# Optimization experiments

Measured on AMD Instinct MI355X. Metric: run time of the kernel, lower is better.

## Reference

```python
import jax, jax.numpy as jnp
import numpy as np

DIM = 256
D_STATE = 64
D_CONV = 4
EXPAND = 2
D_INNER = EXPAND * DIM          # 512
DT_RANK = DIM // 16             # 16, Mamba default dt_rank='auto'
LN_EPS = 1e-5


def setup_inputs() -> dict:
    key = jax.random.key(0)
    ks = jax.random.split(key, 8)
    B, L = 4, 1024
    s = lambda k, shape, fan: jax.random.normal(k, shape, jnp.float32) / np.sqrt(fan).astype(np.float32)
    inp = {}
    inp['x'] = jax.random.normal(ks[0], (B, L, DIM), jnp.float32)
    inp['C_SA'] = jax.random.normal(ks[1], (B, L, D_STATE), jnp.float32)
    # LayerNorm params
    inp['gamma'] = jnp.ones((DIM,), jnp.float32)
    inp['beta'] = jnp.zeros((DIM,), jnp.float32)
    # Mamba params
    inp['W_in'] = s(ks[2], (2 * D_INNER, DIM), DIM)
    inp['conv_w'] = s(ks[3], (D_INNER, 1, D_CONV), D_CONV)   # depthwise causal conv
    inp['conv_b'] = jnp.zeros((D_INNER,), jnp.float32)
    inp['W_x'] = s(ks[4], (DT_RANK + D_STATE, D_INNER), D_INNER)  # -> (dt_low_rank, B_ssm)
    inp['W_dt'] = s(ks[5], (D_INNER, DT_RANK), DT_RANK)
    # softplus-inverse of 0.01 so initial dt ~ 0.01 (Mamba dt init)
    inp['b_dt'] = jnp.log(jnp.expm1(jnp.full((D_INNER,), 0.01, jnp.float32)))
    # S4D-real init: A = -[1..N]
    inp['A_log'] = jnp.log(jnp.broadcast_to(jnp.arange(1, D_STATE + 1, dtype=jnp.float32), (D_INNER, D_STATE)))
    inp['D'] = jnp.ones((D_INNER,), jnp.float32)
    inp['W_out'] = s(ks[6], (DIM, D_INNER), D_INNER)
    return inp


def reference(x, C_SA, gamma, beta, W_in, conv_w, conv_b, W_x, W_dt, b_dt, A_log, D, W_out):
    B, L, _ = x.shape
    # --- LayerNorm ---
    mu = jnp.mean(x, axis=-1, keepdims=True)
    var = jnp.mean(jnp.square(x - mu), axis=-1, keepdims=True)
    xn = (x - mu) * jax.lax.rsqrt(var + LN_EPS) * gamma + beta
    # --- input projection and gate split ---
    xz = xn @ W_in.T                              # [B,L,2*Di]
    u, z = jnp.split(xz, 2, axis=-1)
    # --- causal depthwise conv1d + SiLU ---
    u_c = jax.lax.conv_general_dilated(
        u.transpose(0, 2, 1), conv_w, (1,), [(D_CONV - 1, 0)],
        feature_group_count=D_INNER,
        dimension_numbers=('NCH', 'OIH', 'NCH'))  # [B,Di,L]
    u = jax.nn.silu(u_c.transpose(0, 2, 1) + conv_b)  # [B,L,Di]
    # --- data-dependent SSM params (C comes from C_SA externally) ---
    dbl = u @ W_x.T                               # [B,L,dt_rank+N]
    dt = jax.nn.softplus(dbl[..., :DT_RANK] @ W_dt.T + b_dt)  # [B,L,Di]
    Bs = dbl[..., DT_RANK:]                       # [B,L,N]
    A = -jnp.exp(A_log)                           # [Di,N]
    # --- selective scan over time ---
    def step(h, t):
        dt_t, B_t, C_t, u_t = t                   # [B,Di],[B,N],[B,N],[B,Di]
        dA = jnp.exp(dt_t[..., None] * A)         # [B,Di,N]
        h = dA * h + (dt_t * u_t)[..., None] * B_t[:, None, :]
        y = jnp.einsum('bdn,bn->bd', h, C_t)
        return h, y
    h0 = jnp.zeros((B, D_INNER, D_STATE), x.dtype)
    xs = (dt.transpose(1, 0, 2), Bs.transpose(1, 0, 2),
          C_SA.transpose(1, 0, 2), u.transpose(1, 0, 2))
    _, ys = jax.lax.scan(step, h0, xs)            # ys: [L,B,Di]
    y = ys.transpose(1, 0, 2) + u * D             # skip connection
    y = y * jax.nn.silu(z)                        # gate
    return y @ W_out.T                            # [B,L,dim]
```

## Files before the change

### kernel.cpp

```cpp
#include <hip/hip_runtime.h>
#include <cstdint>
#include <cstddef>

#define B_    4
#define L_    1024
#define DIM_  256
#define DI_   512
#define NTOK  (B_*L_)
#define NC    32
#define CL    (L_/NC)

__device__ __forceinline__ float siluf_(float x){ return x / (1.0f + __expf(-x)); }
__device__ __forceinline__ float softplusf_(float x){
  return (x > 15.0f) ? x : log1pf(__expf(x));
}

__global__ __launch_bounds__(1024) void k_check(const float* __restrict__ A_log,
    int* __restrict__ flag){
  __shared__ int s_ok;
  int tid = threadIdx.x;
  if (tid == 0) s_ok = 1;
  __syncthreads();
  int ok = 1;
  for (int i = tid; i < 512 * 64; i += 1024){
    int n = i & 63;
    float ref = logf((float)(n + 1));
    float v = A_log[i];
    if (fabsf(v - ref) > 1e-5f * fmaxf(1.0f, fabsf(ref))) ok = 0;
  }
  if (!ok) atomicAnd(&s_ok, 0);
  __syncthreads();
  if (tid == 0) *flag = s_ok;
}

__global__ __launch_bounds__(256) void k_ln_stats(const float* __restrict__ x,
    float* __restrict__ stats){
  int tok  = blockIdx.x * 4 + (threadIdx.x >> 6);
  int lane = threadIdx.x & 63;
  float4 v = *(const float4*)(x + (size_t)tok * DIM_ + lane * 4);
  float s  = v.x + v.y + v.z + v.w;
  float sq = v.x*v.x + v.y*v.y + v.z*v.z + v.w*v.w;
  #pragma unroll
  for (int off = 32; off; off >>= 1){
    s  += __shfl_xor(s,  off, 64);
    sq += __shfl_xor(sq, off, 64);
  }
  if (lane == 0){
    float mu = s * (1.0f / DIM_);
    stats[tok*2]   = mu;
    stats[tok*2+1] = rsqrtf(sq * (1.0f / DIM_) - mu*mu + 1e-5f);
  }
}

__global__ __launch_bounds__(256) void k_gemm1(const float* __restrict__ x,
    const float* __restrict__ stats, const float* __restrict__ gamma,
    const float* __restrict__ beta, const float* __restrict__ Win,
    float* __restrict__ xz){
  __shared__ float As[16 * 68];
  __shared__ float Bs[16 * 68];
  int tid = threadIdx.x;
  int mBase = blockIdx.y * 64;
  int nBase = blockIdx.x * 64;
  int tx = tid & 15, ty = tid >> 4;
  int am = tid >> 2, ak = (tid & 3) << 2;
  float mu = stats[(mBase+am)*2], rs = stats[(mBase+am)*2+1];
  float acc[4][4] = {};
  const float* xp = x   + (size_t)(mBase+am)*256 + ak;
  const float* wp = Win + (size_t)(nBase+am)*256 + ak;
  float4 av = *(const float4*)(xp);
  float4 bv = *(const float4*)(wp);
  float4 gv = *(const float4*)(gamma + ak);
  float4 be = *(const float4*)(beta  + ak);
  for (int kt = 0; kt < 256; kt += 16){
    As[(ak+0)*68+am] = (av.x - mu) * rs * gv.x + be.x;
    As[(ak+1)*68+am] = (av.y - mu) * rs * gv.y + be.y;
    As[(ak+2)*68+am] = (av.z - mu) * rs * gv.z + be.z;
    As[(ak+3)*68+am] = (av.w - mu) * rs * gv.w + be.w;
    Bs[(ak+0)*68+am]=bv.x; Bs[(ak+1)*68+am]=bv.y;
    Bs[(ak+2)*68+am]=bv.z; Bs[(ak+3)*68+am]=bv.w;
    __syncthreads();
    float4 avN, bvN, gvN, beN;
    if (kt + 16 < 256){
      avN = *(const float4*)(xp + kt + 16);
      bvN = *(const float4*)(wp + kt + 16);
      gvN = *(const float4*)(gamma + kt + 16 + ak);
      beN = *(const float4*)(beta  + kt + 16 + ak);
    }
    #pragma unroll
    for (int kk = 0; kk < 16; kk++){
      float4 a = *(const float4*)&As[kk*68 + ty*4];
      float4 b = *(const float4*)&Bs[kk*68 + tx*4];
      float ar[4] = {a.x,a.y,a.z,a.w}, br[4] = {b.x,b.y,b.z,b.w};
      #pragma unroll
      for (int i=0;i<4;i++)
        #pragma unroll
        for (int j=0;j<4;j++)
          acc[i][j] += ar[i]*br[j];
    }
    __syncthreads();
    av = avN; bv = bvN; gv = gvN; be = beN;
  }
  #pragma unroll
  for (int i=0;i<4;i++){
    float4 o = make_float4(acc[i][0],acc[i][1],acc[i][2],acc[i][3]);
    *(float4*)(xz + (size_t)(mBase+ty*4+i)*1024 + nBase + tx*4) = o;
  }
}

__global__ __launch_bounds__(256) void k_conv(const float* __restrict__ xz,
    const float* __restrict__ cw, const float* __restrict__ cb,
    float* __restrict__ uc){
  int g = blockIdx.x * 256 + threadIdx.x;
  int d = g & 511;
  int tok = g >> 9;
  int t = tok & (L_ - 1);
  float w0 = cw[d*4+0], w1 = cw[d*4+1], w2 = cw[d*4+2], w3 = cw[d*4+3];
  const float* up = xz + (size_t)tok * 1024 + d;
  float acc = cb[d] + w3 * up[0];
  if (t >= 1) acc += w2 * up[-1 * 1024];
  if (t >= 2) acc += w1 * up[-2 * 1024];
  if (t >= 3) acc += w0 * up[-3 * 1024];
  uc[g] = siluf_(acc);
}

__global__ __launch_bounds__(320) void k_gemm2(const float* __restrict__ uc,
    const float* __restrict__ Wx, float* __restrict__ dbl){
  __shared__ float As[4 * 516];
  int tid = threadIdx.x;
  int mBase = blockIdx.x * 4;
  for (int idx = tid * 4; idx < 4 * 512; idx += 320 * 4){
    int r = idx >> 9, k = idx & 511;
    *(float4*)&As[r * 516 + k] = *(const float4*)(uc + (size_t)(mBase + r) * 512 + k);
  }
  __syncthreads();
  int n = tid >> 2;
  int r = tid & 3;
  const float* arow = &As[r * 516];
  const float* wp = Wx + (size_t)n * 512;
  float acc = 0.f;
  #pragma unroll 8
  for (int k4 = 0; k4 < 512; k4 += 4){
    float4 a = *(const float4*)&arow[k4];
    float4 w = *(const float4*)(wp + k4);
    acc += a.x*w.x + a.y*w.y + a.z*w.z + a.w*w.w;
  }
  dbl[(size_t)(mBase + r) * 80 + n] = acc;
}

__global__ __launch_bounds__(256) void k_dt(const float* __restrict__ dbl,
    const float* __restrict__ Wdt, const float* __restrict__ bdt,
    float* __restrict__ dt){
  int g = blockIdx.x * 256 + threadIdx.x;
  int d = g & 511; int m = g >> 9;
  float acc = bdt[d];
  const float* r = dbl + (size_t)m * 80;
  #pragma unroll
  for (int k = 0; k < 16; k++)
    acc += r[k] * Wdt[d * 16 + k];
  dt[g] = softplusf_(acc);
}

__global__ __launch_bounds__(256, 4) void k_scanA(const float* __restrict__ dt,
    const float* __restrict__ uc, const float* __restrict__ dbl,
    const float* __restrict__ A_log, const int* __restrict__ flagp,
    float* __restrict__ hseg, float* __restrict__ S){
  __shared__ float sB[CL][64];
  __shared__ float sDt[CL][32];
  __shared__ float sU[CL][32];
  int tid  = threadIdx.x;
  int gw   = (blockIdx.x * 256 + tid) >> 6;
  int lane = tid & 63;
  int dsub = lane & 7, ngrp = lane >> 3;
  int grp = gw & 255;
  int c   = gw >> 8;
  int ch  = grp * 8 + dsub;
  int b = ch >> 9, d = ch & 511;
  int tbeg = c * CL;
  int ch0 = ((blockIdx.x * 4) & 255) * 8;
  int d0  = ch0 & 511;
  {
    const float* Bsrc = dbl + (size_t)b * L_ * 80 + (size_t)tbeg * 80 + 16;
    for (int i = tid; i < CL * 16; i += 256){
      int row = i >> 4, col = (i & 15) << 2;
      *(float4*)&sB[row][col] = *(const float4*)(Bsrc + row * 80 + col);
    }
    const float* Dsrc = dt + (size_t)b * L_ * 512 + (size_t)tbeg * 512 + d0;
    const float* Usrc = uc + (size_t)b * L_ * 512 + (size_t)tbeg * 512 + d0;
    int zr = tid >> 3, zc = (tid & 7) << 2;
    *(float4*)&sDt[zr][zc] = *(const float4*)(Dsrc + zr * 512 + zc);
    *(float4*)&sU[zr][zc]  = *(const float4*)(Usrc + zr * 512 + zc);
  }
  __syncthreads();
  int fast = *flagp;
  int lch = (grp & 3) * 8 + dsub;
  float h[8] = {};
  float Ssum = 0.f;
  float st1 = (float)(ngrp * 8 + 1);
  if (fast){
    for (int tt = 0; tt < CL; tt += 4){
      #pragma unroll
      for (int j = 0; j < 4; j++){
        float dtv = sDt[tt+j][lch];
        float uv  = sU[tt+j][lch];
        float4 b0 = *(const float4*)&sB[tt+j][ngrp*8];
        float4 b1 = *(const float4*)&sB[tt+j][ngrp*8+4];
        float sc = dtv * uv;
        Ssum += dtv;
        float e1 = __expf(-dtv);
        float e2 = e1 * e1;
        float e4 = e2 * e2;
        float dA0 = __expf(-dtv * st1);
        float dA1 = dA0 * e1;
        float dA2 = dA0 * e2;
        float dA3 = dA1 * e2;
        h[0] = dA0 * h[0] + sc * b0.x;
        h[1] = dA1 * h[1] + sc * b0.y;
        h[2] = dA2 * h[2] + sc * b0.z;
        h[3] = dA3 * h[3] + sc * b0.w;
        dA0 *= e4; dA1 *= e4; dA2 *= e4; dA3 *= e4;
        h[4] = dA0 * h[4] + sc * b1.x;
        h[5] = dA1 * h[5] + sc * b1.y;
        h[6] = dA2 * h[6] + sc * b1.z;
        h[7] = dA3 * h[7] + sc * b1.w;
      }
    }
  } else {
    float Aa[8];
    float4 a0 = *(const float4*)(A_log + (size_t)d*64 + ngrp*8);
    float4 a1 = *(const float4*)(A_log + (size_t)d*64 + ngrp*8 + 4);
    Aa[0]=-__expf(a0.x); Aa[1]=-__expf(a0.y); Aa[2]=-__expf(a0.z); Aa[3]=-__expf(a0.w);
    Aa[4]=-__expf(a1.x); Aa[5]=-__expf(a1.y); Aa[6]=-__expf(a1.z); Aa[7]=-__expf(a1.w);
    for (int tt = 0; tt < CL; tt += 4){
      #pragma unroll
      for (int j = 0; j < 4; j++){
        float dtv = sDt[tt+j][lch];
        float uv  = sU[tt+j][lch];
        float4 b0 = *(const float4*)&sB[tt+j][ngrp*8];
        float4 b1 = *(const float4*)&sB[tt+j][ngrp*8+4];
        float Bv[8] = {b0.x,b0.y,b0.z,b0.w,b1.x,b1.y,b1.z,b1.w};
        float sc = dtv * uv;
        Ssum += dtv;
        #pragma unroll
        for (int i = 0; i < 8; i++)
          h[i] = __expf(dtv * Aa[i]) * h[i] + sc * Bv[i];
      }
    }
  }
  float* hp = hseg + ((size_t)(c * 2048 + ch)) * 64 + ngrp*8;
  *(float4*)hp     = make_float4(h[0],h[1],h[2],h[3]);
  *(float4*)(hp+4) = make_float4(h[4],h[5],h[6],h[7]);
  if (ngrp == 0) S[c * 2048 + ch] = Ssum;
}

__global__ __launch_bounds__(256) void k_scanB(float* __restrict__ hseg,
    const float* __restrict__ S, const float* __restrict__ A_log,
    const int* __restrict__ flagp){
  int ch   = (blockIdx.x * 256 + threadIdx.x) >> 6;
  int lane = threadIdx.x & 63;
  int d = ch & 511;
  int fast = *flagp;
  float A = fast ? -(float)(lane + 1) : -__expf(A_log[(size_t)d * 64 + lane]);
  float hc = 0.f;
  #pragma unroll 8
  for (int c = 0; c < NC; c++){
    size_t idx = ((size_t)(c * 2048 + ch)) * 64 + lane;
    float hf = hseg[idx];
    hseg[idx] = hc;
    float Sv = S[c * 2048 + ch];
    hc = hf + __expf(A * Sv) * hc;
  }
}

__global__ __launch_bounds__(256, 4) void k_scanC(const float* __restrict__ dt,
    const float* __restrict__ uc, const float* __restrict__ dbl,
    const float* __restrict__ C_SA, const float* __restrict__ A_log,
    const int* __restrict__ flagp,
    const float* __restrict__ hin, const float* __restrict__ xz,
    const float* __restrict__ Dp, float* __restrict__ ys){
  __shared__ float sB[CL][64];
  __shared__ float sC[CL][64];
  __shared__ float sZ[CL][32];
  __shared__ float sDt[CL][32];
  __shared__ float sU[CL][32];
  int tid  = threadIdx.x;
  int gw   = (blockIdx.x * 256 + tid) >> 6;
  int lane = tid & 63;
  int dsub = lane & 7, ngrp = lane >> 3;
  int grp = gw & 255;
  int c   = gw >> 8;
  int ch  = grp * 8 + dsub;
  int b = ch >> 9, d = ch & 511;
  int tbeg = c * CL;
  int ch0 = ((blockIdx.x * 4) & 255) * 8;
  int d0  = ch0 & 511;
  {
    const float* Bsrc = dbl  + (size_t)b * L_ * 80 + (size_t)tbeg * 80 + 16;
    const float* Csrc = C_SA + (size_t)b * L_ * 64 + (size_t)tbeg * 64;
    for (int i = tid; i < CL * 16; i += 256){
      int row = i >> 4, col = (i & 15) << 2;
      *(float4*)&sB[row][col] = *(const float4*)(Bsrc + row * 80 + col);
      *(float4*)&sC[row][col] = *(const float4*)(Csrc + row * 64 + col);
    }
    const float* Zsrc = xz + (size_t)b * L_ * 1024 + (size_t)tbeg * 1024 + 512 + d0;
    const float* Dsrc = dt + (size_t)b * L_ * 512 + (size_t)tbeg * 512 + d0;
    const float* Usrc = uc + (size_t)b * L_ * 512 + (size_t)tbeg * 512 + d0;
    int zr = tid >> 3, zc = (tid & 7) << 2;
    *(float4*)&sZ[zr][zc]  = *(const float4*)(Zsrc + zr * 1024 + zc);
    *(float4*)&sDt[zr][zc] = *(const float4*)(Dsrc + zr * 512 + zc);
    *(float4*)&sU[zr][zc]  = *(const float4*)(Usrc + zr * 512 + zc);
  }
  __syncthreads();
  int fast = *flagp;
  float Dv = Dp[d];
  int lch = (grp & 3) * 8 + dsub;
  float*       yw  = ys + (size_t)b * L_ * 512 + d;
  float h[8];
  {
    const float* hp = hin + ((size_t)(c * 2048 + ch)) * 64 + ngrp*8;
    float4 h0 = *(const float4*)hp;
    float4 h1 = *(const float4*)(hp + 4);
    h[0]=h0.x; h[1]=h0.y; h[2]=h0.z; h[3]=h0.w;
    h[4]=h1.x; h[5]=h1.y; h[6]=h1.z; h[7]=h1.w;
  }
  float st1 = (float)(ngrp * 8 + 1);
  if (fast){
    for (int tt = 0; tt < CL; tt += 4){
      float yp[4], uj[4];
      #pragma unroll
      for (int j = 0; j < 4; j++){
        float dtv = sDt[tt+j][lch];
        float uv  = sU[tt+j][lch];
        uj[j] = uv;
        float4 b0 = *(const float4*)&sB[tt+j][ngrp*8];
        float4 b1 = *(const float4*)&sB[tt+j][ngrp*8+4];
        float4 c0 = *(const float4*)&sC[tt+j][ngrp*8];
        float4 c1 = *(const float4*)&sC[tt+j][ngrp*8+4];
        float sc = dtv * uv;
        float e1 = __expf(-dtv);
        float e2 = e1 * e1;
        float e4 = e2 * e2;
        float dA0 = __expf(-dtv * st1);
        float dA1 = dA0 * e1;
        float dA2 = dA0 * e2;
        float dA3 = dA1 * e2;
        h[0] = dA0 * h[0] + sc * b0.x;
        h[1] = dA1 * h[1] + sc * b0.y;
        h[2] = dA2 * h[2] + sc * b0.z;
        h[3] = dA3 * h[3] + sc * b0.w;
        float y0 = h[0] * c0.x;
        float y1 = h[1] * c0.y;
        float y2 = h[2] * c0.z;
        float y3 = h[3] * c0.w;
        dA0 *= e4; dA1 *= e4; dA2 *= e4; dA3 *= e4;
        h[4] = dA0 * h[4] + sc * b1.x;
        h[5] = dA1 * h[5] + sc * b1.y;
        h[6] = dA2 * h[6] + sc * b1.z;
        h[7] = dA3 * h[7] + sc * b1.w;
        y0 += h[4] * c1.x;
        y1 += h[5] * c1.y;
        y2 += h[6] * c1.z;
        y3 += h[7] * c1.w;
        yp[j] = (y0 + y1) + (y2 + y3);
      }
      #pragma unroll
      for (int off = 8; off < 64; off <<= 1){
        #pragma unroll
        for (int j = 0; j < 4; j++)
          yp[j] += __shfl_xor(yp[j], off, 64);
      }
      if (ngrp == 0){
        #pragma unroll
        for (int j = 0; j < 4; j++){
          float z = sZ[tt+j][lch];
          yw[(size_t)(tbeg+tt+j) * 512] = (yp[j] + uj[j] * Dv) * siluf_(z);
        }
      }
    }
  } else {
    float Aa[8];
    float4 a0 = *(const float4*)(A_log + (size_t)d*64 + ngrp*8);
    float4 a1 = *(const float4*)(A_log + (size_t)d*64 + ngrp*8 + 4);
    Aa[0]=-__expf(a0.x); Aa[1]=-__expf(a0.y); Aa[2]=-__expf(a0.z); Aa[3]=-__expf(a0.w);
    Aa[4]=-__expf(a1.x); Aa[5]=-__expf(a1.y); Aa[6]=-__expf(a1.z); Aa[7]=-__expf(a1.w);
    for (int tt = 0; tt < CL; tt += 4){
      float yp[4], uj[4];
      #pragma unroll
      for (int j = 0; j < 4; j++){
        float dtv = sDt[tt+j][lch];
        float uv  = sU[tt+j][lch];
        uj[j] = uv;
        float4 b0 = *(const float4*)&sB[tt+j][ngrp*8];
        float4 b1 = *(const float4*)&sB[tt+j][ngrp*8+4];
        float4 c0 = *(const float4*)&sC[tt+j][ngrp*8];
        float4 c1 = *(const float4*)&sC[tt+j][ngrp*8+4];
        float sc = dtv * uv;
        h[0] = __expf(dtv * Aa[0]) * h[0] + sc * b0.x;
        h[1] = __expf(dtv * Aa[1]) * h[1] + sc * b0.y;
        h[2] = __expf(dtv * Aa[2]) * h[2] + sc * b0.z;
        h[3] = __expf(dtv * Aa[3]) * h[3] + sc * b0.w;
        float y0 = h[0] * c0.x;
        float y1 = h[1] * c0.y;
        float y2 = h[2] * c0.z;
        float y3 = h[3] * c0.w;
        h[4] = __expf(dtv * Aa[4]) * h[4] + sc * b1.x;
        h[5] = __expf(dtv * Aa[5]) * h[5] + sc * b1.y;
        h[6] = __expf(dtv * Aa[6]) * h[6] + sc * b1.z;
        h[7] = __expf(dtv * Aa[7]) * h[7] + sc * b1.w;
        y0 += h[4] * c1.x;
        y1 += h[5] * c1.y;
        y2 += h[6] * c1.z;
        y3 += h[7] * c1.w;
        yp[j] = (y0 + y1) + (y2 + y3);
      }
      #pragma unroll
      for (int off = 8; off < 64; off <<= 1){
        #pragma unroll
        for (int j = 0; j < 4; j++)
          yp[j] += __shfl_xor(yp[j], off, 64);
      }
      if (ngrp == 0){
        #pragma unroll
        for (int j = 0; j < 4; j++){
          float z = sZ[tt+j][lch];
          yw[(size_t)(tbeg+tt+j) * 512] = (yp[j] + uj[j] * Dv) * siluf_(z);
        }
      }
    }
  }
}

__global__ __launch_bounds__(256) void k_gemm3s(const float* __restrict__ Ag,
    const float* __restrict__ Wout, float* __restrict__ pbuf){
  __shared__ float As[16 * 68];
  __shared__ float Bs[16 * 68];
  int tid = threadIdx.x;
  int nBase = blockIdx.x * 64;
  int mBase = blockIdx.y * 64;
  int kBase = blockIdx.z * 128;
  int tx = tid & 15, ty = tid >> 4;
  int am = tid >> 2, ak = (tid & 3) << 2;
  float acc[4][4] = {};
  const float* ap = Ag   + (size_t)(mBase+am)*512 + ak;
  const float* wp = Wout + (size_t)(nBase+am)*512 + ak;
  float4 av = *(const float4*)(ap + kBase);
  float4 bv = *(const float4*)(wp + kBase);
  for (int kt = kBase; kt < kBase + 128; kt += 16){
    As[(ak+0)*68+am]=av.x; As[(ak+1)*68+am]=av.y;
    As[(ak+2)*68+am]=av.z; As[(ak+3)*68+am]=av.w;
    Bs[(ak+0)*68+am]=bv.x; Bs[(ak+1)*68+am]=bv.y;
    Bs[(ak+2)*68+am]=bv.z; Bs[(ak+3)*68+am]=bv.w;
    __syncthreads();
    float4 avN, bvN;
    if (kt + 16 < kBase + 128){
      avN = *(const float4*)(ap + kt + 16);
      bvN = *(const float4*)(wp + kt + 16);
    }
    #pragma unroll
    for (int kk = 0; kk < 16; kk++){
      float4 a = *(const float4*)&As[kk*68 + ty*4];
      float4 b = *(const float4*)&Bs[kk*68 + tx*4];
      float ar[4] = {a.x,a.y,a.z,a.w}, br[4] = {b.x,b.y,b.z,b.w};
      #pragma unroll
      for (int i=0;i<4;i++)
        #pragma unroll
        for (int j=0;j<4;j++)
          acc[i][j] += ar[i]*br[j];
    }
    __syncthreads();
    av = avN; bv = bvN;
  }
  float* pw = pbuf + (size_t)blockIdx.z * (NTOK * 256);
  #pragma unroll
  for (int i=0;i<4;i++){
    float4 o = make_float4(acc[i][0],acc[i][1],acc[i][2],acc[i][3]);
    *(float4*)(pw + (size_t)(mBase+ty*4+i)*256 + nBase + tx*4) = o;
  }
}

__global__ __launch_bounds__(256) void k_g3red(const float* __restrict__ pbuf,
    float* __restrict__ out){
  int i4 = (blockIdx.x * 256 + threadIdx.x) * 4;
  float4 a = *(const float4*)(pbuf + i4);
  float4 b = *(const float4*)(pbuf + (size_t)NTOK*256   + i4);
  float4 c = *(const float4*)(pbuf + (size_t)NTOK*512   + i4);
  float4 d = *(const float4*)(pbuf + (size_t)NTOK*768   + i4);
  float4 o = make_float4((a.x+b.x)+(c.x+d.x), (a.y+b.y)+(c.y+d.y),
                         (a.z+b.z)+(c.z+d.z), (a.w+b.w)+(c.w+d.w));
  *(float4*)(out + i4) = o;
}

extern "C" void kernel_launch(void* const* d_in, const int* in_sizes, int n_in,
                              void* d_out, int out_size, void* d_ws, size_t ws_size,
                              hipStream_t stream) {
  const float* x      = (const float*)d_in[0];
  const float* C_SA   = (const float*)d_in[1];
  const float* gamma  = (const float*)d_in[2];
  const float* beta   = (const float*)d_in[3];
  const float* W_in   = (const float*)d_in[4];
  const float* conv_w = (const float*)d_in[5];
  const float* conv_b = (const float*)d_in[6];
  const float* W_x    = (const float*)d_in[7];
  const float* W_dt   = (const float*)d_in[8];
  const float* b_dt   = (const float*)d_in[9];
  const float* A_log  = (const float*)d_in[10];
  const float* Dw     = (const float*)d_in[11];
  const float* W_out  = (const float*)d_in[12];
  float* out = (float*)d_out;

  float* ws    = (float*)d_ws;
  float* stats = ws;
  int*   flag  = (int*)(ws + 8192);
  float* xz    = ws    + 16384;
  float* uc    = xz    + 4194304;
  float* dbl   = uc    + 2097152;
  float* dtb   = dbl   + 327680;
  float* hseg  = dtb   + 2097152;
  float* S     = hseg  + 4194304;
  float* ysb   = S     + 65536;
  float* pbuf  = hseg;

  k_check<<<1, 1024, 0, stream>>>(A_log, flag);
  k_ln_stats<<<NTOK/4, 256, 0, stream>>>(x, stats);
  k_gemm1<<<dim3(16, 64), 256, 0, stream>>>(x, stats, gamma, beta, W_in, xz);
  k_conv <<<(NTOK*512)/256, 256, 0, stream>>>(xz, conv_w, conv_b, uc);
  k_gemm2<<<1024, 320, 0, stream>>>(uc, W_x, dbl);
  k_dt   <<<(NTOK*512)/256, 256, 0, stream>>>(dbl, W_dt, b_dt, dtb);
  k_scanA<<<NC*64, 256, 0, stream>>>(dtb, uc, dbl, A_log, flag, hseg, S);
  k_scanB<<<512, 256, 0, stream>>>(hseg, S, A_log, flag);
  k_scanC<<<NC*64, 256, 0, stream>>>(dtb, uc, dbl, C_SA, A_log, flag, hseg, xz, Dw, ysb);
  k_gemm3s<<<dim3(4, 64, 4), 256, 0, stream>>>(ysb, W_out, pbuf);
  k_g3red<<<NTOK*256/1024, 256, 0, stream>>>(pbuf, out);
}
```

Baseline: 242.8 us.

## Retile x-projection GEMM into register-blocked warp tiles with split-K shuffle reduction

Rewrites the u @ W_x^T kernel so each 64-lane wavefront computes an 8-token by 8-output tile. K is split across 8 lane groups and the partial sums are combined with xor shuffles. The old version staged 4 rows in shared memory and had each thread do a full 512-long dot product while reloading W_x rows from global memory. The new scheme gets register reuse of the activation chunks across 8 outputs and drops shared memory and the barrier, at the cost of higher register pressure and only one lane in eight doing the stores.

```diff
diff --git a/kernel.cpp b/kernel.cpp
--- a/kernel.cpp
+++ b/kernel.cpp
@@ -123,28 +123,48 @@
   uc[g] = siluf_(acc);
 }
 
-__global__ __launch_bounds__(320) void k_gemm2(const float* __restrict__ uc,
+__global__ __launch_bounds__(256) void k_gemm2(const float* __restrict__ uc,
     const float* __restrict__ Wx, float* __restrict__ dbl){
-  __shared__ float As[4 * 516];
-  int tid = threadIdx.x;
-  int mBase = blockIdx.x * 4;
-  for (int idx = tid * 4; idx < 4 * 512; idx += 320 * 4){
-    int r = idx >> 9, k = idx & 511;
-    *(float4*)&As[r * 516 + k] = *(const float4*)(uc + (size_t)(mBase + r) * 512 + k);
-  }
-  __syncthreads();
-  int n = tid >> 2;
-  int r = tid & 3;
-  const float* arow = &As[r * 516];
-  const float* wp = Wx + (size_t)n * 512;
-  float acc = 0.f;
-  #pragma unroll 8
-  for (int k4 = 0; k4 < 512; k4 += 4){
-    float4 a = *(const float4*)&arow[k4];
-    float4 w = *(const float4*)(wp + k4);
-    acc += a.x*w.x + a.y*w.y + a.z*w.z + a.w*w.w;
-  }
-  dbl[(size_t)(mBase + r) * 80 + n] = acc;
+  int tid  = threadIdx.x;
+  int w    = blockIdx.x * 4 + (tid >> 6);
+  int lane = tid & 63;
+  int tg = w / 10;
+  int ng = w - tg * 10;
+  int ts = lane >> 3;
+  int ko = lane & 7;
+  int m  = tg * 8 + ts;
+  const float4* ap = (const float4*)(uc + (size_t)m * 512 + ko * 64);
+  const float*  wb = Wx + (size_t)(ng * 8) * 512 + ko * 64;
+  float pn[8] = {};
+  #pragma unroll
+  for (int half = 0; half < 2; half++){
+    float4 a[8];
+    #pragma unroll
+    for (int i = 0; i < 8; i++) a[i] = ap[half*8 + i];
+    #pragma unroll
+    for (int n = 0; n < 8; n++){
+      const float4* wp = (const float4*)(wb + (size_t)n * 512) + half*8;
+      float4 w0 = wp[0], w1 = wp[1], w2 = wp[2], w3 = wp[3];
+      float4 w4 = wp[4], w5 = wp[5], w6 = wp[6], w7 = wp[7];
+      float s0 = a[0].x*w0.x + a[0].y*w0.y + a[0].z*w0.z + a[0].w*w0.w
+               + a[4].x*w4.x + a[4].y*w4.y + a[4].z*w4.z + a[4].w*w4.w;
+      float s1 = a[1].x*w1.x + a[1].y*w1.y + a[1].z*w1.z + a[1].w*w1.w
+               + a[5].x*w5.x + a[5].y*w5.y + a[5].z*w5.z + a[5].w*w5.w;
+      float s2 = a[2].x*w2.x + a[2].y*w2.y + a[2].z*w2.z + a[2].w*w2.w
+               + a[6].x*w6.x + a[6].y*w6.y + a[6].z*w6.z + a[6].w*w6.w;
+      float s3 = a[3].x*w3.x + a[3].y*w3.y + a[3].z*w3.z + a[3].w*w3.w
+               + a[7].x*w7.x + a[7].y*w7.y + a[7].z*w7.z + a[7].w*w7.w;
+      pn[n] += (s0 + s1) + (s2 + s3);
+    }
+  }
+  #pragma unroll
+  for (int n = 0; n < 8; n++){
+    float p = pn[n];
+    p += __shfl_xor(p, 1, 64);
+    p += __shfl_xor(p, 2, 64);
+    p += __shfl_xor(p, 4, 64);
+    if (ko == 0) dbl[(size_t)m * 80 + ng * 8 + n] = p;
+  }
 }
 
 __global__ __launch_bounds__(256) void k_dt(const float* __restrict__ dbl,
@@ -523,7 +543,7 @@
   k_ln_stats<<<NTOK/4, 256, 0, stream>>>(x, stats);
   k_gemm1<<<dim3(16, 64), 256, 0, stream>>>(x, stats, gamma, beta, W_in, xz);
   k_conv <<<(NTOK*512)/256, 256, 0, stream>>>(xz, conv_w, conv_b, uc);
-  k_gemm2<<<1024, 320, 0, stream>>>(uc, W_x, dbl);
+  k_gemm2<<<1280, 256, 0, stream>>>(uc, W_x, dbl);
   k_dt   <<<(NTOK*512)/256, 256, 0, stream>>>(dbl, W_dt, b_dt, dtb);
   k_scanA<<<NC*64, 256, 0, stream>>>(dtb, uc, dbl, A_log, flag, hseg, S);
   k_scanB<<<512, 256, 0, stream>>>(hseg, S, A_log, flag);
```

New measurement: 327.3 us. 34.8% more time.

## Replace x_proj GEMM with split-K register-tiled kernel plus reduction

Applied to the files above, without the earlier changes.

Replaces the per-row x_proj GEMM, which streamed W_x from global memory for every 4 rows, with a shared-memory tiled kernel. Each thread computes a 4x5 register tile over a 64x80 output tile, and K is split 16 ways across blocks. The partial sums go to a scratch buffer that aliases hseg and are summed by a new reduction kernel. This adds a second launch and roughly 21 MB of partial-sum traffic in exchange for much better reuse of both operands.

```diff
diff --git a/kernel.cpp b/kernel.cpp
--- a/kernel.cpp
+++ b/kernel.cpp
@@ -123,28 +123,62 @@
   uc[g] = siluf_(acc);
 }
 
-__global__ __launch_bounds__(320) void k_gemm2(const float* __restrict__ uc,
-    const float* __restrict__ Wx, float* __restrict__ dbl){
-  __shared__ float As[4 * 516];
+__global__ __launch_bounds__(256) void k_gemm2s(const float* __restrict__ uc,
+    const float* __restrict__ Wx, float* __restrict__ pbuf2){
+  __shared__ float As[16 * 68];
+  __shared__ float Bs[16 * 84];
   int tid = threadIdx.x;
-  int mBase = blockIdx.x * 4;
-  for (int idx = tid * 4; idx < 4 * 512; idx += 320 * 4){
-    int r = idx >> 9, k = idx & 511;
-    *(float4*)&As[r * 516 + k] = *(const float4*)(uc + (size_t)(mBase + r) * 512 + k);
-  }
-  __syncthreads();
-  int n = tid >> 2;
-  int r = tid & 3;
-  const float* arow = &As[r * 516];
-  const float* wp = Wx + (size_t)n * 512;
-  float acc = 0.f;
-  #pragma unroll 8
-  for (int k4 = 0; k4 < 512; k4 += 4){
-    float4 a = *(const float4*)&arow[k4];
-    float4 w = *(const float4*)(wp + k4);
-    acc += a.x*w.x + a.y*w.y + a.z*w.z + a.w*w.w;
-  }
-  dbl[(size_t)(mBase + r) * 80 + n] = acc;
+  int mBase = blockIdx.y * 64;
+  int kBase = blockIdx.x * 32;
+  int tx = tid & 15, ty = tid >> 4;
+  int am = tid >> 2, ak = (tid & 3) << 2;
+  float acc[4][5] = {};
+  for (int kt = kBase; kt < kBase + 32; kt += 16){
+    {
+      float4 av = *(const float4*)(uc + (size_t)(mBase+am)*512 + kt + ak);
+      As[(ak+0)*68+am]=av.x; As[(ak+1)*68+am]=av.y;
+      As[(ak+2)*68+am]=av.z; As[(ak+3)*68+am]=av.w;
+    }
+    for (int i = tid; i < 320; i += 256){
+      int row = i >> 2, c4 = (i & 3) << 2;
+      float4 wv = *(const float4*)(Wx + (size_t)row*512 + kt + c4);
+      Bs[(c4+0)*84+row]=wv.x; Bs[(c4+1)*84+row]=wv.y;
+      Bs[(c4+2)*84+row]=wv.z; Bs[(c4+3)*84+row]=wv.w;
+    }
+    __syncthreads();
+    #pragma unroll
+    for (int kk = 0; kk < 16; kk++){
+      float4 a = *(const float4*)&As[kk*68 + ty*4];
+      float ar[4] = {a.x,a.y,a.z,a.w};
+      const float* bp = &Bs[kk*84 + tx*5];
+      float br[5] = {bp[0], bp[1], bp[2], bp[3], bp[4]};
+      #pragma unroll
+      for (int i=0;i<4;i++)
+        #pragma unroll
+        for (int j=0;j<5;j++)
+          acc[i][j] += ar[i]*br[j];
+    }
+    __syncthreads();
+  }
+  float* pw = pbuf2 + (size_t)blockIdx.x * (NTOK * 80);
+  #pragma unroll
+  for (int i=0;i<4;i++){
+    float* row = pw + (size_t)(mBase+ty*4+i)*80 + tx*5;
+    #pragma unroll
+    for (int j=0;j<5;j++) row[j] = acc[i][j];
+  }
+}
+
+__global__ __launch_bounds__(256) void k_g2red(const float* __restrict__ pbuf2,
+    float* __restrict__ dbl){
+  int i4 = (blockIdx.x * 256 + threadIdx.x) * 4;
+  float4 s = make_float4(0.f, 0.f, 0.f, 0.f);
+  #pragma unroll
+  for (int z = 0; z < 16; z++){
+    float4 p = *(const float4*)(pbuf2 + (size_t)z * (NTOK * 80) + i4);
+    s.x += p.x; s.y += p.y; s.z += p.z; s.w += p.w;
+  }
+  *(float4*)(dbl + i4) = s;
 }
 
 __global__ __launch_bounds__(256) void k_dt(const float* __restrict__ dbl,
@@ -518,12 +552,14 @@
   float* S     = hseg  + 4194304;
   float* ysb   = S     + 65536;
   float* pbuf  = hseg;
+  float* pbuf2 = hseg;
 
   k_check<<<1, 1024, 0, stream>>>(A_log, flag);
   k_ln_stats<<<NTOK/4, 256, 0, stream>>>(x, stats);
   k_gemm1<<<dim3(16, 64), 256, 0, stream>>>(x, stats, gamma, beta, W_in, xz);
   k_conv <<<(NTOK*512)/256, 256, 0, stream>>>(xz, conv_w, conv_b, uc);
-  k_gemm2<<<1024, 320, 0, stream>>>(uc, W_x, dbl);
+  k_gemm2s<<<dim3(16, 64), 256, 0, stream>>>(uc, W_x, pbuf2);
+  k_g2red<<<(NTOK*80)/1024, 256, 0, stream>>>(pbuf2, dbl);
   k_dt   <<<(NTOK*512)/256, 256, 0, stream>>>(dbl, W_dt, b_dt, dtb);
   k_scanA<<<NC*64, 256, 0, stream>>>(dtb, uc, dbl, A_log, flag, hseg, S);
   k_scanB<<<512, 256, 0, stream>>>(hseg, S, A_log, flag);
```

Measured after the change: 246.1 us. About the same (+1.4%).
